# Optimization experiments

Hardware: AMD Instinct MI355X
Metric: run time of the kernel (lower is better)

The kernel has to match this reference:

```python
import jax, jax.numpy as jnp
import numpy as np


def _bilinear2d(uv, table):
    """Bilinear lookup with wrap addressing; sigmoid non-linearity applied per
    corner (normalize=True in SpatialGrid2D), matching training-time forward.
    uv: (N,2) in [0,1); table: (U,V,L). Returns (N,L)."""
    U, V, _ = table.shape
    su = uv[:, 0] * U
    sv = uv[:, 1] * V
    u0 = jnp.floor(su)
    v0 = jnp.floor(sv)
    fu = (su - u0)[:, None]  # fractional weights, (N,1)
    fv = (sv - v0)[:, None]
    u0i = jnp.mod(u0.astype(jnp.int32), U)
    v0i = jnp.mod(v0.astype(jnp.int32), V)
    u1i = jnp.mod(u0i + 1, U)
    v1i = jnp.mod(v0i + 1, V)
    t00 = jax.nn.sigmoid(table[u0i, v0i])
    t10 = jax.nn.sigmoid(table[u1i, v0i])
    t01 = jax.nn.sigmoid(table[u0i, v1i])
    t11 = jax.nn.sigmoid(table[u1i, v1i])
    return (t00 * (1 - fu) + t10 * fu) * (1 - fv) + (t01 * (1 - fu) + t11 * fu) * fv


def setup_inputs() -> dict:
    key = jax.random.key(0)
    k1, k2, k3 = jax.random.split(key, 3)
    N = 2048 * 2048  # query points (one per pixel)
    RES = 520        # grid0 resolution from nativeResolution=4096, compression=6
    x = jax.random.uniform(k1, (N, 2), dtype=jnp.float32)
    grid1_table = jax.random.normal(k2, (RES * 4, RES * 4, 2), dtype=jnp.float32)
    grid0_table = jax.random.normal(k3, (RES, RES, 3), dtype=jnp.float32)
    return {"x": x, "grid1_table": grid1_table, "grid0_table": grid0_table}


def reference(x, grid1_table, grid0_table):
    # forward: grid0(grid1(x)) -- chained bilinear indirection lookups
    key = _bilinear2d(x, grid1_table)   # (N,2) indirected uv coords in (0,1)
    return _bilinear2d(key, grid0_table)  # (N,3) decoded RGB
```

## Files before the change

kernel.cpp:

```cpp
#include <hip/hip_runtime.h>
#include <math.h>


typedef float f32x2 __attribute__((ext_vector_type(2)));
typedef float f32x4 __attribute__((ext_vector_type(4)));
typedef float f32x4u __attribute__((ext_vector_type(4), aligned(4)));
typedef float f32x2u __attribute__((ext_vector_type(2), aligned(4)));

__device__ __forceinline__ float mul_rn_nocontract(float a, float b) {
    float r;
    asm("v_mul_f32 %0, %1, %2" : "=v"(r) : "v"(a), "v"(b));
    return r;
}

__device__ __forceinline__ float sigmoid_ref(float t) {
    float e = expf(-t);
    return (float)(1.0 / (1.0 + (double)e));
}

__global__ void __launch_bounds__(256) pack_fused_kernel(
    const float* __restrict__ g1, float* __restrict__ pk, int U1)
{
    int v = blockIdx.x * 256 + threadIdx.x;
    int u = blockIdx.y;
    if (v >= U1) return;
    int v1 = v + 1; if (v1 >= U1) v1 = 0;
    int u1 = u + 1; if (u1 >= U1) u1 = 0;

    const f32x2* g = reinterpret_cast<const f32x2*>(g1);
    size_t ru0 = (size_t)u  * U1;
    size_t ru1 = (size_t)u1 * U1;
    f32x2 t00 = g[ru0 + v];
    f32x2 t01 = g[ru0 + v1];
    f32x2 t10 = g[ru1 + v];
    f32x2 t11 = g[ru1 + v1];

    f32x4 lo, hi;
    lo.x = sigmoid_ref(t00.x); lo.y = sigmoid_ref(t00.y);
    lo.z = sigmoid_ref(t01.x); lo.w = sigmoid_ref(t01.y);
    hi.x = sigmoid_ref(t10.x); hi.y = sigmoid_ref(t10.y);
    hi.z = sigmoid_ref(t11.x); hi.w = sigmoid_ref(t11.y);

    f32x4* o = reinterpret_cast<f32x4*>(pk + (ru0 + v) * 8);
    o[0] = lo;
    o[1] = hi;
}

__global__ void __launch_bounds__(256) sigmoid_table_kernel(
    const float4* __restrict__ in, float4* __restrict__ out, int n4)
{
    int i = blockIdx.x * blockDim.x + threadIdx.x;
    if (i >= n4) return;
    float4 v = in[i];
    float4 r;
    r.x = sigmoid_ref(v.x);
    r.y = sigmoid_ref(v.y);
    r.z = sigmoid_ref(v.z);
    r.w = sigmoid_ref(v.w);
    out[i] = r;
}

__global__ void __launch_bounds__(256) query_packed_kernel(
    const float* __restrict__ x,
    const float* __restrict__ pk,
    const float* __restrict__ s0,
    float* __restrict__ out,
    int N, int U1, int U0)
{
    int i = blockIdx.x * blockDim.x + threadIdx.x;
    if (i >= N) return;

    f32x2 uv = __builtin_nontemporal_load(
        reinterpret_cast<const f32x2*>(x) + i);

    float fU1 = (float)U1;
    float su = mul_rn_nocontract(uv.x, fU1);
    float sv = mul_rn_nocontract(uv.y, fU1);
    float u0f = floorf(su), v0f = floorf(sv);
    float fu = su - u0f;
    float fv = sv - v0f;
    int u0 = (int)u0f % U1; if (u0 < 0) u0 += U1;
    int v0 = (int)v0f % U1; if (v0 < 0) v0 += U1;

    const float4* cell = reinterpret_cast<const float4*>(pk)
                       + (size_t)(u0 * U1 + v0) * 2;
    float4 lo = cell[0];
    float4 hi = cell[1];

    float omfu = 1.0f - fu, omfv = 1.0f - fv;
    float kx = (lo.x * omfu + hi.x * fu) * omfv
             + (lo.z * omfu + hi.z * fu) * fv;
    float ky = (lo.y * omfu + hi.y * fu) * omfv
             + (lo.w * omfu + hi.w * fu) * fv;

    float fU0 = (float)U0;
    float su2 = mul_rn_nocontract(kx, fU0);
    float sv2 = mul_rn_nocontract(ky, fU0);
    float u0f2 = floorf(su2), v0f2 = floorf(sv2);
    float fu2 = su2 - u0f2, fv2 = sv2 - v0f2;
    int p0 = (int)u0f2 % U0; if (p0 < 0) p0 += U0;
    int q0 = (int)v0f2 % U0; if (q0 < 0) q0 += U0;
    int p1 = p0 + 1; if (p1 >= U0) p1 = 0;
    int q1 = q0 + 1; if (q1 >= U0) q1 = 0;

    float a00, a01, a02, a10, a11, a12;
    float b00v, b01v, b02v, b10v, b11v, b12v;
    if (q1 != 0) {
        const float* r0p = s0 + (size_t)(p0 * U0 + q0) * 3;
        f32x4u h0 = *reinterpret_cast<const f32x4u*>(r0p);
        f32x2u h1 = *reinterpret_cast<const f32x2u*>(r0p + 4);
        a00 = h0.x; a01 = h0.y; a02 = h0.z;
        a10 = h0.w; a11 = h1.x; a12 = h1.y;
        const float* r1p = s0 + (size_t)(p1 * U0 + q0) * 3;
        f32x4u h2 = *reinterpret_cast<const f32x4u*>(r1p);
        f32x2u h3 = *reinterpret_cast<const f32x2u*>(r1p + 4);
        b00v = h2.x; b01v = h2.y; b02v = h2.z;
        b10v = h2.w; b11v = h3.x; b12v = h3.y;
    } else {
        int c00 = (p0 * U0 + q0) * 3, c01 = (p0 * U0 + q1) * 3;
        int c10 = (p1 * U0 + q0) * 3, c11 = (p1 * U0 + q1) * 3;
        a00 = s0[c00+0]; a01 = s0[c00+1]; a02 = s0[c00+2];
        a10 = s0[c01+0]; a11 = s0[c01+1]; a12 = s0[c01+2];
        b00v = s0[c10+0]; b01v = s0[c10+1]; b02v = s0[c10+2];
        b10v = s0[c11+0]; b11v = s0[c11+1]; b12v = s0[c11+2];
    }

    float omfu2 = 1.0f - fu2, omfv2 = 1.0f - fv2;
    float r0 = (a00 * omfu2 + b00v * fu2) * omfv2
             + (a10 * omfu2 + b10v * fu2) * fv2;
    float r1 = (a01 * omfu2 + b01v * fu2) * omfv2
             + (a11 * omfu2 + b11v * fu2) * fv2;
    float r2 = (a02 * omfu2 + b02v * fu2) * omfv2
             + (a12 * omfu2 + b12v * fu2) * fv2;
    out[3*i+0] = r0; out[3*i+1] = r1; out[3*i+2] = r2;
}

__global__ void __launch_bounds__(256) query_direct_kernel(
    const float* __restrict__ x,
    const float* __restrict__ g1,
    const float* __restrict__ s0,
    float* __restrict__ out,
    int N, int U1, int U0)
{
    int i = blockIdx.x * blockDim.x + threadIdx.x;
    if (i >= N) return;

    f32x2 uv = __builtin_nontemporal_load(
        reinterpret_cast<const f32x2*>(x) + i);

    float fU1 = (float)U1;
    float su = mul_rn_nocontract(uv.x, fU1);
    float sv = mul_rn_nocontract(uv.y, fU1);
    float u0f = floorf(su), v0f = floorf(sv);
    float fu = su - u0f, fv = sv - v0f;
    int u0 = (int)u0f % U1; if (u0 < 0) u0 += U1;
    int v0 = (int)v0f % U1; if (v0 < 0) v0 += U1;
    int u1 = u0 + 1; if (u1 >= U1) u1 = 0;
    int v1 = v0 + 1; if (v1 >= U1) v1 = 0;

    const f32x2* g = reinterpret_cast<const f32x2*>(g1);
    const f32x2* row0 = g + (size_t)u0 * U1;
    const f32x2* row1 = g + (size_t)u1 * U1;
    f32x2 t00 = row0[v0];
    f32x2 t01 = row0[v1];
    f32x2 t10 = row1[v0];
    f32x2 t11 = row1[v1];

    float a00x = sigmoid_ref(t00.x), a00y = sigmoid_ref(t00.y);
    float a10x = sigmoid_ref(t10.x), a10y = sigmoid_ref(t10.y);
    float a01x = sigmoid_ref(t01.x), a01y = sigmoid_ref(t01.y);
    float a11x = sigmoid_ref(t11.x), a11y = sigmoid_ref(t11.y);

    float omfu = 1.0f - fu, omfv = 1.0f - fv;
    float kx = (a00x * omfu + a10x * fu) * omfv
             + (a01x * omfu + a11x * fu) * fv;
    float ky = (a00y * omfu + a10y * fu) * omfv
             + (a01y * omfu + a11y * fu) * fv;

    float fU0 = (float)U0;
    float su2 = mul_rn_nocontract(kx, fU0);
    float sv2 = mul_rn_nocontract(ky, fU0);
    float u0f2 = floorf(su2), v0f2 = floorf(sv2);
    float fu2 = su2 - u0f2, fv2 = sv2 - v0f2;
    int p0 = (int)u0f2 % U0; if (p0 < 0) p0 += U0;
    int q0 = (int)v0f2 % U0; if (q0 < 0) q0 += U0;
    int p1 = p0 + 1; if (p1 >= U0) p1 = 0;
    int q1 = q0 + 1; if (q1 >= U0) q1 = 0;
    int b00 = (p0 * U0 + q0) * 3, b10 = (p1 * U0 + q0) * 3;
    int b01 = (p0 * U0 + q1) * 3, b11 = (p1 * U0 + q1) * 3;
    float omfu2 = 1.0f - fu2, omfv2 = 1.0f - fv2;
    float r0 = (s0[b00+0] * omfu2 + s0[b10+0] * fu2) * omfv2
             + (s0[b01+0] * omfu2 + s0[b11+0] * fu2) * fv2;
    float r1 = (s0[b00+1] * omfu2 + s0[b10+1] * fu2) * omfv2
             + (s0[b01+1] * omfu2 + s0[b11+1] * fu2) * fv2;
    float r2 = (s0[b00+2] * omfu2 + s0[b10+2] * fu2) * omfv2
             + (s0[b01+2] * omfu2 + s0[b11+2] * fu2) * fv2;
    out[3*i+0] = r0; out[3*i+1] = r1; out[3*i+2] = r2;
}

__global__ void __launch_bounds__(256) query_kernel_fallback(
    const float* __restrict__ x,
    const float* __restrict__ g1,
    const float* __restrict__ g0,
    float* __restrict__ out,
    int N, int U1, int U0)
{
    int i = blockIdx.x * blockDim.x + threadIdx.x;
    if (i >= N) return;
    float2 uv = reinterpret_cast<const float2*>(x)[i];
    float fU1 = (float)U1;
    float su = mul_rn_nocontract(uv.x, fU1);
    float sv = mul_rn_nocontract(uv.y, fU1);
    float u0f = floorf(su), v0f = floorf(sv);
    float fu = su - u0f, fv = sv - v0f;
    int u0 = (int)u0f % U1; if (u0 < 0) u0 += U1;
    int v0 = (int)v0f % U1; if (v0 < 0) v0 += U1;
    int u1 = u0 + 1; if (u1 >= U1) u1 = 0;
    int v1 = v0 + 1; if (v1 >= U1) v1 = 0;
    const float2* g1v = reinterpret_cast<const float2*>(g1);
    float2 t00 = g1v[u0 * U1 + v0];
    float2 t10 = g1v[u1 * U1 + v0];
    float2 t01 = g1v[u0 * U1 + v1];
    float2 t11 = g1v[u1 * U1 + v1];
    float a00x = sigmoid_ref(t00.x), a00y = sigmoid_ref(t00.y);
    float a10x = sigmoid_ref(t10.x), a10y = sigmoid_ref(t10.y);
    float a01x = sigmoid_ref(t01.x), a01y = sigmoid_ref(t01.y);
    float a11x = sigmoid_ref(t11.x), a11y = sigmoid_ref(t11.y);
    float omfu = 1.0f - fu, omfv = 1.0f - fv;
    float kx = (a00x * omfu + a10x * fu) * omfv + (a01x * omfu + a11x * fu) * fv;
    float ky = (a00y * omfu + a10y * fu) * omfv + (a01y * omfu + a11y * fu) * fv;
    float fU0 = (float)U0;
    float su2 = mul_rn_nocontract(kx, fU0);
    float sv2 = mul_rn_nocontract(ky, fU0);
    float u0f2 = floorf(su2), v0f2 = floorf(sv2);
    float fu2 = su2 - u0f2, fv2 = sv2 - v0f2;
    int p0 = (int)u0f2 % U0; if (p0 < 0) p0 += U0;
    int q0 = (int)v0f2 % U0; if (q0 < 0) q0 += U0;
    int p1 = p0 + 1; if (p1 >= U0) p1 = 0;
    int q1 = q0 + 1; if (q1 >= U0) q1 = 0;
    int b00 = (p0 * U0 + q0) * 3, b10 = (p1 * U0 + q0) * 3;
    int b01 = (p0 * U0 + q1) * 3, b11 = (p1 * U0 + q1) * 3;
    float omfu2 = 1.0f - fu2, omfv2 = 1.0f - fv2;
    float r0 = (sigmoid_ref(g0[b00+0]) * omfu2 + sigmoid_ref(g0[b10+0]) * fu2) * omfv2
             + (sigmoid_ref(g0[b01+0]) * omfu2 + sigmoid_ref(g0[b11+0]) * fu2) * fv2;
    float r1 = (sigmoid_ref(g0[b00+1]) * omfu2 + sigmoid_ref(g0[b10+1]) * fu2) * omfv2
             + (sigmoid_ref(g0[b01+1]) * omfu2 + sigmoid_ref(g0[b11+1]) * fu2) * fv2;
    float r2 = (sigmoid_ref(g0[b00+2]) * omfu2 + sigmoid_ref(g0[b10+2]) * fu2) * omfv2
             + (sigmoid_ref(g0[b01+2]) * omfu2 + sigmoid_ref(g0[b11+2]) * fu2) * fv2;
    out[3*i+0] = r0; out[3*i+1] = r1; out[3*i+2] = r2;
}

extern "C" void kernel_launch(void* const* d_in, const int* in_sizes, int n_in,
                              void* d_out, int out_size, void* d_ws, size_t ws_size,
                              hipStream_t stream) {
    const float* x  = (const float*)d_in[0];
    const float* g1 = (const float*)d_in[1];
    const float* g0 = (const float*)d_in[2];
    float* out = (float*)d_out;

    int N = in_sizes[0] / 2;
    long long n1 = in_sizes[1];
    long long n0 = in_sizes[2];
    int U1 = (int)(sqrt((double)(n1 / 2)) + 0.5);
    int U0 = (int)(sqrt((double)(n0 / 3)) + 0.5);
    long long ncells1 = (long long)U1 * U1;

    int block = 256;
    size_t need_packed = ((size_t)ncells1 * 8 + (size_t)n0) * sizeof(float);
    size_t need_s0     = (size_t)n0 * sizeof(float);

    if (ws_size >= need_packed && (n0 % 4) == 0) {
        float* pk = (float*)d_ws;
        float* s0 = pk + ncells1 * 8;
        int n0_4 = (int)(n0 / 4);
        dim3 pgrid((U1 + block - 1) / block, U1);
        pack_fused_kernel<<<pgrid, block, 0, stream>>>(g1, pk, U1);
        sigmoid_table_kernel<<<(n0_4 + block - 1) / block, block, 0, stream>>>(
            (const float4*)g0, (float4*)s0, n0_4);
        query_packed_kernel<<<(N + block - 1) / block, block, 0, stream>>>(
            x, pk, s0, out, N, U1, U0);
    } else if (ws_size >= need_s0 && (n0 % 4) == 0) {
        float* s0 = (float*)d_ws;
        int n0_4 = (int)(n0 / 4);
        sigmoid_table_kernel<<<(n0_4 + block - 1) / block, block, 0, stream>>>(
            (const float4*)g0, (float4*)s0, n0_4);
        query_direct_kernel<<<(N + block - 1) / block, block, 0, stream>>>(
            x, g1, s0, out, N, U1, U0);
    } else {
        query_kernel_fallback<<<(N + block - 1) / block, block, 0, stream>>>(
            x, g1, g0, out, N, U1, U0);
    }
}
```

Before: 249.9 us.

## Pack grid1 as row pairs and compute sigmoid at query time

The grid1 table was previously packed into 32-byte cells holding all four corners with sigmoid already applied. It is now packed into 16-byte row-pair entries holding raw values from rows u and u+1, and the query kernel reads two adjacent entries and applies sigmoid itself. This halves the packed table size and the bytes written by the pack kernel, which eases DRAM and cache pressure. The cost is eight double-precision sigmoids per query and two gathers instead of one contiguous 32-byte load.

Result: faster. 237.3 us (-5.0%).

```diff
diff --git a/kernel.cpp b/kernel.cpp
--- a/kernel.cpp
+++ b/kernel.cpp
@@ -18,32 +18,20 @@
     return (float)(1.0 / (1.0 + (double)e));
 }
 
-__global__ void __launch_bounds__(256) pack_fused_kernel(
-    const float* __restrict__ g1, float* __restrict__ pk, int U1)
+__global__ void __launch_bounds__(256) rowpair_pack_kernel(
+    const float* __restrict__ g1, float* __restrict__ rp, int U1)
 {
     int v = blockIdx.x * 256 + threadIdx.x;
     int u = blockIdx.y;
     if (v >= U1) return;
-    int v1 = v + 1; if (v1 >= U1) v1 = 0;
     int u1 = u + 1; if (u1 >= U1) u1 = 0;
 
     const f32x2* g = reinterpret_cast<const f32x2*>(g1);
-    size_t ru0 = (size_t)u  * U1;
-    size_t ru1 = (size_t)u1 * U1;
-    f32x2 t00 = g[ru0 + v];
-    f32x2 t01 = g[ru0 + v1];
-    f32x2 t10 = g[ru1 + v];
-    f32x2 t11 = g[ru1 + v1];
-
-    f32x4 lo, hi;
-    lo.x = sigmoid_ref(t00.x); lo.y = sigmoid_ref(t00.y);
-    lo.z = sigmoid_ref(t01.x); lo.w = sigmoid_ref(t01.y);
-    hi.x = sigmoid_ref(t10.x); hi.y = sigmoid_ref(t10.y);
-    hi.z = sigmoid_ref(t11.x); hi.w = sigmoid_ref(t11.y);
-
-    f32x4* o = reinterpret_cast<f32x4*>(pk + (ru0 + v) * 8);
-    o[0] = lo;
-    o[1] = hi;
+    f32x2 a = g[(size_t)u  * U1 + v];
+    f32x2 b = g[(size_t)u1 * U1 + v];
+    f32x4 e;
+    e.x = a.x; e.y = a.y; e.z = b.x; e.w = b.y;
+    reinterpret_cast<f32x4*>(rp)[(size_t)u * U1 + v] = e;
 }
 
 __global__ void __launch_bounds__(256) sigmoid_table_kernel(
@@ -60,9 +48,9 @@
     out[i] = r;
 }
 
-__global__ void __launch_bounds__(256) query_packed_kernel(
+__global__ void __launch_bounds__(256) query_rowpair_kernel(
     const float* __restrict__ x,
-    const float* __restrict__ pk,
+    const float* __restrict__ rp,
     const float* __restrict__ s0,
     float* __restrict__ out,
     int N, int U1, int U0)
@@ -81,17 +69,23 @@
     float fv = sv - v0f;
     int u0 = (int)u0f % U1; if (u0 < 0) u0 += U1;
     int v0 = (int)v0f % U1; if (v0 < 0) v0 += U1;
-
-    const float4* cell = reinterpret_cast<const float4*>(pk)
-                       + (size_t)(u0 * U1 + v0) * 2;
-    float4 lo = cell[0];
-    float4 hi = cell[1];
+    int v1 = v0 + 1; if (v1 >= U1) v1 = 0;
+
+    const f32x4* rpv = reinterpret_cast<const f32x4*>(rp)
+                     + (size_t)u0 * U1;
+    f32x4 e0 = rpv[v0];
+    f32x4 e1 = rpv[v1];
+
+    float a00x = sigmoid_ref(e0.x), a00y = sigmoid_ref(e0.y);
+    float a10x = sigmoid_ref(e0.z), a10y = sigmoid_ref(e0.w);
+    float a01x = sigmoid_ref(e1.x), a01y = sigmoid_ref(e1.y);
+    float a11x = sigmoid_ref(e1.z), a11y = sigmoid_ref(e1.w);
 
     float omfu = 1.0f - fu, omfv = 1.0f - fv;
-    float kx = (lo.x * omfu + hi.x * fu) * omfv
-             + (lo.z * omfu + hi.z * fu) * fv;
-    float ky = (lo.y * omfu + hi.y * fu) * omfv
-             + (lo.w * omfu + hi.w * fu) * fv;
+    float kx = (a00x * omfu + a10x * fu) * omfv
+             + (a01x * omfu + a11x * fu) * fv;
+    float ky = (a00y * omfu + a10y * fu) * omfv
+             + (a01y * omfu + a11y * fu) * fv;
 
     float fU0 = (float)U0;
     float su2 = mul_rn_nocontract(kx, fU0);
@@ -266,19 +260,19 @@
     long long ncells1 = (long long)U1 * U1;
 
     int block = 256;
-    size_t need_packed = ((size_t)ncells1 * 8 + (size_t)n0) * sizeof(float);
-    size_t need_s0     = (size_t)n0 * sizeof(float);
-
-    if (ws_size >= need_packed && (n0 % 4) == 0) {
-        float* pk = (float*)d_ws;
-        float* s0 = pk + ncells1 * 8;
+    size_t need_rowpair = ((size_t)ncells1 * 4 + (size_t)n0) * sizeof(float);
+    size_t need_s0      = (size_t)n0 * sizeof(float);
+
+    if (ws_size >= need_rowpair && (n0 % 4) == 0) {
+        float* rp = (float*)d_ws;
+        float* s0 = rp + ncells1 * 4;
         int n0_4 = (int)(n0 / 4);
         dim3 pgrid((U1 + block - 1) / block, U1);
-        pack_fused_kernel<<<pgrid, block, 0, stream>>>(g1, pk, U1);
+        rowpair_pack_kernel<<<pgrid, block, 0, stream>>>(g1, rp, U1);
         sigmoid_table_kernel<<<(n0_4 + block - 1) / block, block, 0, stream>>>(
             (const float4*)g0, (float4*)s0, n0_4);
-        query_packed_kernel<<<(N + block - 1) / block, block, 0, stream>>>(
-            x, pk, s0, out, N, U1, U0);
+        query_rowpair_kernel<<<(N + block - 1) / block, block, 0, stream>>>(
+            x, rp, s0, out, N, U1, U0);
     } else if (ws_size >= need_s0 && (n0 % 4) == 0) {
         float* s0 = (float*)d_ws;
         int n0_4 = (int)(n0 / 4);
```
